# Optimization experiments

Measured on AMD Instinct MI355X. Metric: run time of the kernel, lower is better.

The kernel has to match this reference:

```python
import jax, jax.numpy as jnp
import numpy as np

N = 100000
E = 1600000
H = 128
R = 200
NB = 16  # num_bases (blocks)


def _softplus(x):
    return jax.nn.softplus(x)


def bdd_rel_conv(h, src, dst, etype, norm, W, loop_w, bias, act):
    # W: (R, NB, si, so); block-diagonal decomposition RelGraphConv (DGL semantics)
    nb, si, so = W.shape[1], W.shape[2], W.shape[3]
    h_src = h[src].reshape(-1, nb, si)          # gather per-edge src feats
    W_e = W[etype]                               # (E, nb, si, so) per-edge blocks
    msg = jnp.einsum('ebi,ebio->ebo', h_src, W_e).reshape(-1, nb * so)
    msg = msg * norm                             # edge norm, (E,1)
    agg = jax.ops.segment_sum(msg, dst, num_segments=h.shape[0])
    out = agg + bias + h @ loop_w                # bias + self-loop
    return act(out)


def setup_inputs() -> dict:
    key = jax.random.key(0)
    ks = jax.random.split(key, 12)
    node_ids = jnp.arange(N, dtype=jnp.int32)
    src = jax.random.randint(ks[0], (E,), 0, N)
    dst = jax.random.randint(ks[1], (E,), 0, N)
    etype = jax.random.randint(ks[2], (E,), 0, R)
    norm = jax.random.uniform(ks[3], (E, 1), dtype=jnp.float32)
    emb = jax.random.normal(ks[4], (N, H), dtype=jnp.float32)
    si = H // NB
    W1 = jax.random.normal(ks[5], (R, NB, si, si), dtype=jnp.float32) * 0.05
    loop1 = jax.random.normal(ks[6], (H, H), dtype=jnp.float32) * 0.05
    b1 = jnp.zeros((H,), dtype=jnp.float32)
    W2 = jax.random.normal(ks[7], (R, NB, si, 2 * si), dtype=jnp.float32) * 0.05
    loop2 = jax.random.normal(ks[8], (H, 2 * H), dtype=jnp.float32) * 0.05
    b2 = jnp.zeros((2 * H,), dtype=jnp.float32)
    eps = jax.random.normal(ks[9], (N, H), dtype=jnp.float32)
    return {"node_ids": node_ids, "src": src, "dst": dst, "etype": etype,
            "norm": norm, "emb": emb, "W1": W1, "loop1": loop1, "b1": b1,
            "W2": W2, "loop2": loop2, "b2": b2, "eps": eps}


def reference(node_ids, src, dst, etype, norm, emb, W1, loop1, b1, W2, loop2, b2, eps):
    h = emb[node_ids]                                  # EmbeddingLayer
    h = bdd_rel_conv(h, src, dst, etype, norm, W1, loop1, b1, jax.nn.relu)
    h = bdd_rel_conv(h, src, dst, etype, norm, W2, loop2, b2, lambda x: x)
    m, hv = jnp.split(h, 2, axis=-1)                   # gaussian_parameters
    v = _softplus(hv) + 1e-8
    z = m + jnp.sqrt(v) * eps                          # sample_gaussian
    return z
```

## Files before the change

### kernel.cpp

```cpp
#include <hip/hip_runtime.h>
#include <math.h>

#define N_NODES 100000
#define N_EDGES 1600000
#define HDIM 128
#define NBLK 16
#define NREL 200
#define NW_AGG 8192
#define NT 8

typedef unsigned short ushort_t;
typedef unsigned int uint_t;
typedef _Float16 h2 __attribute__((ext_vector_type(2)));

__device__ __forceinline__ ushort_t f2h(float f) {
  _Float16 h = (_Float16)f;
  return __builtin_bit_cast(unsigned short, h);
}
__device__ __forceinline__ float h2f(ushort_t b) {
  return (float)__builtin_bit_cast(_Float16, b);
}

#if defined(__has_builtin) && __has_builtin(__builtin_amdgcn_fdot2)
#define FDOT2(accv, au, bu)                                                    \
  accv = __builtin_amdgcn_fdot2(__builtin_bit_cast(h2, au),                    \
                                __builtin_bit_cast(h2, bu), accv, false);
#else
#define FDOT2(accv, au, bu)                                                    \
  {                                                                            \
    h2 av_ = __builtin_bit_cast(h2, au);                                       \
    h2 bv_ = __builtin_bit_cast(h2, bu);                                       \
    accv = fmaf((float)av_[0], (float)bv_[0], accv);                           \
    accv = fmaf((float)av_[1], (float)bv_[1], accv);                           \
  }
#endif

#if defined(__has_builtin) && __has_builtin(__builtin_amdgcn_global_load_lds)
#define HAVE_GLL 1
#else
#define HAVE_GLL 0
#endif

#if HAVE_GLL
#define STAGE_H(HSRC, SMEMW)                                                   \
  {                                                                            \
    _Pragma("unroll") for (int i_ = 0; i_ < 8; ++i_) {                         \
      int ei_ = (i_ << 2) + (l >> 4);                                          \
      if (ei_ >= m) ei_ = m - 1;                                               \
      int ss_ = __shfl(r.x, ei_);                                              \
      const ushort_t* gsrc_ = HSRC + ((long)ss_ << 7) + ((l & 15) << 3);       \
      __builtin_amdgcn_global_load_lds(                                        \
          (const __attribute__((address_space(1))) unsigned int*)gsrc_,        \
          (__attribute__((address_space(3))) unsigned int*)&SMEMW[i_ << 9],    \
          16, 0, 0);                                                           \
    }                                                                          \
    asm volatile("s_waitcnt vmcnt(0)" ::: "memory");                           \
  }
#else
#define STAGE_H(HSRC, SMEMW)                                                   \
  {                                                                            \
    _Pragma("unroll") for (int i_ = 0; i_ < 8; ++i_) {                         \
      int ei_ = (i_ << 2) + (l >> 4);                                          \
      if (ei_ >= m) ei_ = m - 1;                                               \
      int ss_ = __shfl(r.x, ei_);                                              \
      const ushort_t* gsrc_ = HSRC + ((long)ss_ << 7) + ((l & 15) << 3);       \
      uint4 t_ = *(const uint4*)gsrc_;                                         \
      *(uint4*)&SMEMW[(i_ << 9) + (l << 3)] = t_;                              \
    }                                                                          \
  }
#endif

__global__ __launch_bounds__(256) void hist_deg(const int* __restrict__ dst,
                                                int* __restrict__ deg) {
  int e = blockIdx.x * 256 + threadIdx.x;
  if (e < N_EDGES) atomicAdd(&deg[dst[e]], 1);
}

__global__ __launch_bounds__(1024) void scan_offsets(const int* __restrict__ deg,
                                                     int* __restrict__ offsets) {
  __shared__ int wsum[16];
  __shared__ int carry_s;
  int tid = threadIdx.x, lane = tid & 63, wid = tid >> 6;
  if (tid == 0) carry_s = 0;
  __syncthreads();
  for (int base = 0; base < N_NODES; base += 1024) {
    int i = base + tid;
    int v = (i < N_NODES) ? deg[i] : 0;
    int x = v;
#pragma unroll
    for (int s = 1; s < 64; s <<= 1) {
      int t = __shfl_up(x, s);
      if (lane >= s) x += t;
    }
    if (lane == 63) wsum[wid] = x;
    __syncthreads();
    if (wid == 0) {
      int y = (lane < 16) ? wsum[lane] : 0;
#pragma unroll
      for (int s = 1; s < 16; s <<= 1) {
        int t = __shfl_up(y, s);
        if (lane >= s) y += t;
      }
      if (lane < 16) wsum[lane] = y;
    }
    __syncthreads();
    int carry = carry_s;
    int wbase = (wid > 0) ? wsum[wid - 1] : 0;
    if (i < N_NODES) offsets[i] = carry + wbase + (x - v);
    __syncthreads();
    if (tid == 0) carry_s = carry + wsum[15];
    __syncthreads();
  }
  if (tid == 0) offsets[N_NODES] = carry_s;
}

__global__ __launch_bounds__(256) void scatter_rec(
    const int* __restrict__ src, const int* __restrict__ dst,
    const int* __restrict__ etype, const float* __restrict__ norm,
    const int* __restrict__ offsets, int* __restrict__ cursor,
    int4* __restrict__ rec) {
  int e = blockIdx.x * 256 + threadIdx.x;
  if (e >= N_EDGES) return;
  int d = dst[e];
  int pos = offsets[d] + atomicAdd(&cursor[d], 1);
  rec[pos] = make_int4(src[e], etype[e], __float_as_int(norm[e]), 0);
}

__global__ __launch_bounds__(256) void calc_ranges(const int* __restrict__ offsets,
                                                   int* __restrict__ ranges) {
  int w = blockIdx.x * 256 + threadIdx.x;
  if (w > NW_AGG) return;
  if (w == NW_AGG) {
    ranges[w] = N_NODES;
    return;
  }
  long t = ((long)w * N_EDGES + NW_AGG - 1) / NW_AGG;
  int lo = 0, hi = N_NODES;
  while (lo < hi) {
    int mid = (lo + hi) >> 1;
    if ((long)offsets[mid] >= t) hi = mid;
    else lo = mid + 1;
  }
  ranges[w] = lo;
}

__global__ __launch_bounds__(256) void conv_h0(const int* __restrict__ node_ids,
                                               const float* __restrict__ emb,
                                               ushort_t* __restrict__ h0h) {
  long gid = (long)blockIdx.x * 256 + threadIdx.x;
  if (gid >= (long)N_NODES * HDIM) return;
  int n = (int)(gid >> 7);
  int o = (int)(gid & 127);
  h0h[gid] = f2h(emb[(long)node_ids[n] * HDIM + o]);
}

__global__ __launch_bounds__(256) void conv_w1(const float* __restrict__ W,
                                               ushort_t* __restrict__ Wh) {
  int idx = blockIdx.x * 256 + threadIdx.x;
  if (idx >= NREL * NBLK * 64) return;
  int rb = idx >> 6, i = (idx >> 3) & 7, o = idx & 7;
  int g = o >> 1, c = o & 1, ip = i >> 1, hi = i & 1;
  Wh[(((rb * 4 + g) * 2 + c) * 4 + ip) * 2 + hi] = f2h(W[idx]);
}

__global__ __launch_bounds__(256) void conv_w2(const float* __restrict__ W,
                                               ushort_t* __restrict__ Wh) {
  int idx = blockIdx.x * 256 + threadIdx.x;
  if (idx >= NREL * NBLK * 128) return;
  int rb = idx >> 7, i = (idx >> 4) & 7, o = idx & 15;
  int g = o >> 2, c = o & 3, ip = i >> 1, hi = i & 1;
  Wh[(((rb * 4 + g) * 4 + c) * 4 + ip) * 2 + hi] = f2h(W[idx]);
}

__global__ __launch_bounds__(256, 4) void agg_layer1(
    const int4* __restrict__ rec, const int* __restrict__ offsets,
    const int* __restrict__ ranges, const ushort_t* __restrict__ h0h,
    const ushort_t* __restrict__ Wh, float* __restrict__ agg) {
  __shared__ __align__(16) ushort_t smem[4][4096];
  int w = blockIdx.x * 4 + (threadIdx.x >> 6);
  int l = threadIdx.x & 63;
  int wid = threadIdx.x >> 6;
  int lo = ranges[w], hi = ranges[w + 1];
  if (lo >= hi) return;
  const ushort_t* Wl = Wh + (size_t)l * 16;
  int hoff = (l >> 2) << 3;
  int estart = offsets[lo];
  int ecnt = offsets[hi] - estart;
  int cur = lo;
  int next_b = offsets[lo + 1];
  int e = estart;
  float ac0 = 0.f, ac1 = 0.f;

#define L1_FLUSH                                                               \
  {                                                                            \
    float2 res = {ac0, ac1};                                                   \
    *(float2*)(agg + (long)cur * HDIM + (l << 1)) = res;                       \
    ac0 = ac1 = 0.f;                                                           \
    ++cur;                                                                     \
    next_b = offsets[cur + 1];                                                 \
  }

  for (int c0 = 0; c0 < ecnt; c0 += 32) {
    int m = min(32, ecnt - c0);
    int4 r = make_int4(0, 0, 0, 0);
    if (l < m) r = rec[estart + c0 + l];
    STAGE_H(h0h, smem[wid])
    for (int k = 0; k < m; ++k) {
      while (e == next_b) L1_FLUSH
      int wy_ = __shfl(r.y, k);
      float nn_ = __uint_as_float((uint_t)__shfl(r.z, k));
      const uint4* Wp_ = (const uint4*)(Wl + (size_t)wy_ * 1024);
      uint4 q0_ = Wp_[0], q1_ = Wp_[1];
      uint4 u = *(const uint4*)&smem[wid][(k << 7) + hoff];
      float p0 = 0.f, p1 = 0.f;
      FDOT2(p0, u.x, q0_.x) FDOT2(p0, u.y, q0_.y)
      FDOT2(p0, u.z, q0_.z) FDOT2(p0, u.w, q0_.w)
      FDOT2(p1, u.x, q1_.x) FDOT2(p1, u.y, q1_.y)
      FDOT2(p1, u.z, q1_.z) FDOT2(p1, u.w, q1_.w)
      ac0 = fmaf(p0, nn_, ac0);
      ac1 = fmaf(p1, nn_, ac1);
      ++e;
    }
  }
  while (cur < hi) {
    float2 res = {ac0, ac1};
    *(float2*)(agg + (long)cur * HDIM + (l << 1)) = res;
    ac0 = ac1 = 0.f;
    ++cur;
  }
#undef L1_FLUSH
}

__global__ __launch_bounds__(256, 4) void agg_layer2(
    const int4* __restrict__ rec, const int* __restrict__ offsets,
    const int* __restrict__ ranges, const ushort_t* __restrict__ h1h,
    const ushort_t* __restrict__ Wh, float* __restrict__ agg) {
  __shared__ __align__(16) ushort_t smem[4][4096];
  int w = blockIdx.x * 4 + (threadIdx.x >> 6);
  int l = threadIdx.x & 63;
  int wid = threadIdx.x >> 6;
  int lo = ranges[w], hi = ranges[w + 1];
  if (lo >= hi) return;
  const ushort_t* Wl = Wh + (size_t)l * 32;
  int hoff = (l >> 2) << 3;
  int estart = offsets[lo];
  int ecnt = offsets[hi] - estart;
  int cur = lo;
  int next_b = offsets[lo + 1];
  int e = estart;
  float ax = 0.f, ay = 0.f, az = 0.f, aw = 0.f;

#define L2_FLUSH                                                               \
  {                                                                            \
    float4 res = {ax, ay, az, aw};                                             \
    *(float4*)(agg + (long)cur * 256 + (l << 2)) = res;                        \
    ax = ay = az = aw = 0.f;                                                   \
    ++cur;                                                                     \
    next_b = offsets[cur + 1];                                                 \
  }

  for (int c0 = 0; c0 < ecnt; c0 += 32) {
    int m = min(32, ecnt - c0);
    int4 r = make_int4(0, 0, 0, 0);
    if (l < m) r = rec[estart + c0 + l];
    STAGE_H(h1h, smem[wid])
    for (int k = 0; k < m; ++k) {
      while (e == next_b) L2_FLUSH
      int wy_ = __shfl(r.y, k);
      float nn_ = __uint_as_float((uint_t)__shfl(r.z, k));
      const uint4* Wp_ = (const uint4*)(Wl + (size_t)wy_ * 2048);
      uint4 q0_ = Wp_[0], q1_ = Wp_[1], q2_ = Wp_[2], q3_ = Wp_[3];
      uint4 u = *(const uint4*)&smem[wid][(k << 7) + hoff];
      float px = 0.f, py = 0.f, pz = 0.f, pw = 0.f;
      FDOT2(px, u.x, q0_.x) FDOT2(px, u.y, q0_.y)
      FDOT2(px, u.z, q0_.z) FDOT2(px, u.w, q0_.w)
      FDOT2(py, u.x, q1_.x) FDOT2(py, u.y, q1_.y)
      FDOT2(py, u.z, q1_.z) FDOT2(py, u.w, q1_.w)
      FDOT2(pz, u.x, q2_.x) FDOT2(pz, u.y, q2_.y)
      FDOT2(pz, u.z, q2_.z) FDOT2(pz, u.w, q2_.w)
      FDOT2(pw, u.x, q3_.x) FDOT2(pw, u.y, q3_.y)
      FDOT2(pw, u.z, q3_.z) FDOT2(pw, u.w, q3_.w)
      ax = fmaf(px, nn_, ax);
      ay = fmaf(py, nn_, ay);
      az = fmaf(pz, nn_, az);
      aw = fmaf(pw, nn_, aw);
      ++e;
    }
  }
  while (cur < hi) {
    float4 res = {ax, ay, az, aw};
    *(float4*)(agg + (long)cur * 256 + (l << 2)) = res;
    ax = ay = az = aw = 0.f;
    ++cur;
  }
#undef L2_FLUSH
}

__global__ __launch_bounds__(256) void node_layer1(
    const ushort_t* __restrict__ h0h, const float* __restrict__ loop1,
    const float* __restrict__ agg1, const float* __restrict__ bias,
    ushort_t* __restrict__ h1h) {
  __shared__ __align__(8) ushort_t Lh[128 * 130];
  __shared__ __align__(8) ushort_t hs[NT * 128];
  int tid = threadIdx.x;
  for (int t = 0; t < 64; ++t) {
    int flat = t * 256 + tid;
    int i = flat >> 7, o = flat & 127;
    Lh[o * 130 + i] = f2h(loop1[i * 128 + o]);
  }
  __syncthreads();
  int o = tid & 127;
  int g = tid >> 7;
  for (int grp = blockIdx.x; grp < N_NODES / NT; grp += gridDim.x) {
    int n0 = grp * NT;
    __syncthreads();
    for (int t = 0; t < 4; ++t) {
      int flat = t * 256 + tid;
      int j = flat >> 7, i = flat & 127;
      hs[j * 128 + i] = h0h[(long)(n0 + j) * 128 + i];
    }
    __syncthreads();
    float acc[4] = {0.f, 0.f, 0.f, 0.f};
    const ushort_t* Lo = &Lh[o * 130];
    const ushort_t* hb = &hs[(g * 4) * 128];
    for (int i = 0; i < 128; i += 4) {
      uint_t lv01 = *(const uint_t*)&Lo[i];
      uint_t lv23 = *(const uint_t*)&Lo[i + 2];
#pragma unroll
      for (int j = 0; j < 4; ++j) {
        uint2 hj = *(const uint2*)&hb[j * 128 + i];
        FDOT2(acc[j], hj.x, lv01)
        FDOT2(acc[j], hj.y, lv23)
      }
    }
    float bo = bias[o];
#pragma unroll
    for (int j = 0; j < 4; ++j) {
      int n = n0 + g * 4 + j;
      float v = acc[j] + bo + agg1[(long)n * 128 + o];
      h1h[(long)n * 128 + o] = f2h(fmaxf(v, 0.f));
    }
  }
}

__global__ __launch_bounds__(256) void node_layer2f(
    const ushort_t* __restrict__ h1h, const float* __restrict__ loop2,
    const float* __restrict__ agg2, const float* __restrict__ bias2,
    const float* __restrict__ eps, float* __restrict__ out) {
  __shared__ __align__(8) ushort_t Lh[256 * 130];
  __shared__ __align__(8) ushort_t hs[NT * 128];
  __shared__ float spbuf[NT * 128];
  int o = threadIdx.x;
  for (int t = 0; t < 128; ++t) {
    int flat = t * 256 + o;
    int i = flat >> 8, c = flat & 255;
    Lh[c * 130 + i] = f2h(loop2[i * 256 + c]);
  }
  __syncthreads();
  for (int grp = blockIdx.x; grp < N_NODES / NT; grp += gridDim.x) {
    int n0 = grp * NT;
    __syncthreads();
    for (int t = 0; t < 4; ++t) {
      int flat = t * 256 + o;
      int j = flat >> 7, i = flat & 127;
      hs[j * 128 + i] = h1h[(long)(n0 + j) * 128 + i];
    }
    __syncthreads();
    float acc[NT] = {0.f, 0.f, 0.f, 0.f, 0.f, 0.f, 0.f, 0.f};
    const ushort_t* Lo = &Lh[o * 130];
    for (int i = 0; i < 128; i += 4) {
      uint_t lv01 = *(const uint_t*)&Lo[i];
      uint_t lv23 = *(const uint_t*)&Lo[i + 2];
#pragma unroll
      for (int j = 0; j < NT; ++j) {
        uint2 hj = *(const uint2*)&hs[j * 128 + i];
        FDOT2(acc[j], hj.x, lv01)
        FDOT2(acc[j], hj.y, lv23)
      }
    }
    float bo = bias2[o];
    if (o >= 128) {
      int oc = o - 128;
#pragma unroll
      for (int j = 0; j < NT; ++j) {
        float hv = acc[j] + bo + agg2[(long)(n0 + j) * 256 + o];
        float sp = fmaxf(hv, 0.f) + log1pf(expf(-fabsf(hv)));
        spbuf[j * 128 + oc] = sqrtf(sp + 1e-8f);
      }
    }
    __syncthreads();
    if (o < 128) {
#pragma unroll
      for (int j = 0; j < NT; ++j) {
        float mval = acc[j] + bo + agg2[(long)(n0 + j) * 256 + o];
        long off2 = (long)(n0 + j) * 128 + o;
        out[off2] = mval + spbuf[j * 128 + o] * eps[off2];
      }
    }
  }
}

extern "C" void kernel_launch(void* const* d_in, const int* in_sizes, int n_in,
                              void* d_out, int out_size, void* d_ws, size_t ws_size,
                              hipStream_t stream) {
  const int* node_ids = (const int*)d_in[0];
  const int* src      = (const int*)d_in[1];
  const int* dst      = (const int*)d_in[2];
  const int* etype    = (const int*)d_in[3];
  const float* norm   = (const float*)d_in[4];
  const float* emb    = (const float*)d_in[5];
  const float* W1     = (const float*)d_in[6];
  const float* loop1  = (const float*)d_in[7];
  const float* b1     = (const float*)d_in[8];
  const float* W2     = (const float*)d_in[9];
  const float* loop2  = (const float*)d_in[10];
  const float* b2     = (const float*)d_in[11];
  const float* eps    = (const float*)d_in[12];
  float* out = (float*)d_out;

  char* ws = (char*)d_ws;
  size_t off = 0;
  int* deg       = (int*)(ws + off); off += (size_t)N_NODES * 4;
  int* offsets   = (int*)(ws + off); off += (size_t)(N_NODES + 1) * 4;
  int* cursor    = (int*)(ws + off); off += (size_t)N_NODES * 4;
  int* ranges    = (int*)(ws + off); off += (size_t)(NW_AGG + 1) * 4;
  int4* rec      = (int4*)(ws + off); off += (size_t)N_EDGES * 16;
  float* agg2    = (float*)(ws + off); off += (size_t)N_NODES * 256 * 4;
  ushort_t* h0h  = (ushort_t*)(ws + off); off += (size_t)N_NODES * HDIM * 2;
  ushort_t* h1h  = (ushort_t*)(ws + off); off += (size_t)N_NODES * HDIM * 2;
  ushort_t* Wh1  = (ushort_t*)(ws + off); off += (size_t)NREL * NBLK * 64 * 2;
  ushort_t* Wh2  = (ushort_t*)(ws + off); off += (size_t)NREL * NBLK * 128 * 2;
  float* agg1 = out;

  hipMemsetAsync(deg, 0, (size_t)N_NODES * 4, stream);
  hipMemsetAsync(cursor, 0, (size_t)N_NODES * 4, stream);
  hist_deg<<<(N_EDGES + 255) / 256, 256, 0, stream>>>(dst, deg);
  conv_w1<<<(NREL * NBLK * 64 + 255) / 256, 256, 0, stream>>>(W1, Wh1);
  conv_w2<<<(NREL * NBLK * 128 + 255) / 256, 256, 0, stream>>>(W2, Wh2);
  scan_offsets<<<1, 1024, 0, stream>>>(deg, offsets);
  calc_ranges<<<(NW_AGG + 256) / 256, 256, 0, stream>>>(offsets, ranges);
  scatter_rec<<<(N_EDGES + 255) / 256, 256, 0, stream>>>(src, dst, etype, norm,
                                                         offsets, cursor, rec);
  conv_h0<<<(N_NODES * HDIM + 255) / 256, 256, 0, stream>>>(node_ids, emb, h0h);

  agg_layer1<<<NW_AGG / 4, 256, 0, stream>>>(rec, offsets, ranges, h0h, Wh1, agg1);
  node_layer1<<<1024, 256, 0, stream>>>(h0h, loop1, agg1, b1, h1h);

  agg_layer2<<<NW_AGG / 4, 256, 0, stream>>>(rec, offsets, ranges, h1h, Wh2, agg2);
  node_layer2f<<<512, 256, 0, stream>>>(h1h, loop2, agg2, b2, eps, out);
}
```

Measured before the change: 1.151 ms.

## Sort edges by relation, materialize per-edge messages, then reduce per destination node

Adds a second edge ordering grouped by relation type, so the message kernels load each relation's weight block once into registers and process 64-edge tiles. Each kernel writes fp16 messages into a per-edge buffer indexed by the edge's CSR position. The node kernels then sum those messages per destination while applying the self-loop and activation. This removes the per-edge weight gather from the old destination-ordered aggregation, at the cost of writing and re-reading a large message buffer (up to 800 MB) and adding extra histogram, scan and scatter passes. The new path runs only if the workspace is large enough; otherwise the old path is kept.

```diff
diff --git a/kernel.cpp b/kernel.cpp
--- a/kernel.cpp
+++ b/kernel.cpp
@@ -7,6 +7,7 @@
 #define NBLK 16
 #define NREL 200
 #define NW_AGG 8192
+#define TILE_E 64
 #define NT 8
 
 typedef unsigned short ushort_t;
@@ -42,7 +43,7 @@
 #endif
 
 #if HAVE_GLL
-#define STAGE_H(HSRC, SMEMW)                                                   \
+#define STAGE_H32(HSRC, SMEMW)                                                 \
   {                                                                            \
     _Pragma("unroll") for (int i_ = 0; i_ < 8; ++i_) {                         \
       int ei_ = (i_ << 2) + (l >> 4);                                          \
@@ -57,7 +58,7 @@
     asm volatile("s_waitcnt vmcnt(0)" ::: "memory");                           \
   }
 #else
-#define STAGE_H(HSRC, SMEMW)                                                   \
+#define STAGE_H32(HSRC, SMEMW)                                                 \
   {                                                                            \
     _Pragma("unroll") for (int i_ = 0; i_ < 8; ++i_) {                         \
       int ei_ = (i_ << 2) + (l >> 4);                                          \
@@ -70,10 +71,45 @@
   }
 #endif
 
+#if HAVE_GLL
+#define STAGE16R(HSRC, SLABP, RR, MM, LL)                                      \
+  {                                                                            \
+    _Pragma("unroll") for (int i_ = 0; i_ < 4; ++i_) {                         \
+      int ei_ = (i_ << 2) + (LL >> 4);                                         \
+      if (ei_ >= MM) ei_ = MM - 1;                                             \
+      int ss_ = __shfl(RR.x, ei_);                                             \
+      const ushort_t* gsrc_ = HSRC + ((long)ss_ << 7) + ((LL & 15) << 3);      \
+      __builtin_amdgcn_global_load_lds(                                        \
+          (const __attribute__((address_space(1))) unsigned int*)gsrc_,        \
+          (__attribute__((address_space(3))) unsigned int*)&SLABP[i_ << 9],    \
+          16, 0, 0);                                                           \
+    }                                                                          \
+    asm volatile("s_waitcnt vmcnt(0)" ::: "memory");                           \
+  }
+#else
+#define STAGE16R(HSRC, SLABP, RR, MM, LL)                                      \
+  {                                                                            \
+    _Pragma("unroll") for (int i_ = 0; i_ < 4; ++i_) {                         \
+      int ei_ = (i_ << 2) + (LL >> 4);                                         \
+      if (ei_ >= MM) ei_ = MM - 1;                                             \
+      int ss_ = __shfl(RR.x, ei_);                                             \
+      const ushort_t* gsrc_ = HSRC + ((long)ss_ << 7) + ((LL & 15) << 3);      \
+      uint4 t_ = *(const uint4*)gsrc_;                                         \
+      *(uint4*)&SLABP[(i_ << 9) + (LL << 3)] = t_;                             \
+    }                                                                          \
+  }
+#endif
+
 __global__ __launch_bounds__(256) void hist_deg(const int* __restrict__ dst,
                                                 int* __restrict__ deg) {
   int e = blockIdx.x * 256 + threadIdx.x;
   if (e < N_EDGES) atomicAdd(&deg[dst[e]], 1);
+}
+
+__global__ __launch_bounds__(256) void hist_rel(const int* __restrict__ etype,
+                                                int* __restrict__ cnt2) {
+  int e = blockIdx.x * 256 + threadIdx.x;
+  if (e < N_EDGES) atomicAdd(&cnt2[etype[e]], 1);
 }
 
 __global__ __launch_bounds__(1024) void scan_offsets(const int* __restrict__ deg,
@@ -114,6 +150,37 @@
   if (tid == 0) offsets[N_NODES] = carry_s;
 }
 
+__global__ __launch_bounds__(256) void scan_rel(const int* __restrict__ cnt2,
+                                                int* __restrict__ off2,
+                                                int* __restrict__ tileOff) {
+  __shared__ int b1[256], b2[256];
+  int t = threadIdx.x;
+  int c = (t < NREL) ? cnt2[t] : 0;
+  int tc = (c + TILE_E - 1) / TILE_E;
+  int x1 = c, x2 = tc;
+  b1[t] = x1;
+  b2[t] = x2;
+  __syncthreads();
+  for (int s = 1; s < 256; s <<= 1) {
+    int a1 = (t >= s) ? b1[t - s] : 0;
+    int a2 = (t >= s) ? b2[t - s] : 0;
+    __syncthreads();
+    x1 += a1;
+    x2 += a2;
+    b1[t] = x1;
+    b2[t] = x2;
+    __syncthreads();
+  }
+  if (t < NREL) {
+    off2[t] = x1 - c;
+    tileOff[t] = x2 - tc;
+  }
+  if (t == NREL - 1) {
+    off2[NREL] = x1;
+    tileOff[NREL] = x2;
+  }
+}
+
 __global__ __launch_bounds__(256) void scatter_rec(
     const int* __restrict__ src, const int* __restrict__ dst,
     const int* __restrict__ etype, const float* __restrict__ norm,
@@ -124,6 +191,21 @@
   int d = dst[e];
   int pos = offsets[d] + atomicAdd(&cursor[d], 1);
   rec[pos] = make_int4(src[e], etype[e], __float_as_int(norm[e]), 0);
+}
+
+__global__ __launch_bounds__(256) void scatter2(
+    const int* __restrict__ src, const int* __restrict__ dst,
+    const int* __restrict__ etype, const float* __restrict__ norm,
+    const int* __restrict__ offsets, int* __restrict__ cursor,
+    const int* __restrict__ off2, int* __restrict__ cur2,
+    int4* __restrict__ rec2) {
+  int e = blockIdx.x * 256 + threadIdx.x;
+  if (e >= N_EDGES) return;
+  int d = dst[e];
+  int pc = offsets[d] + atomicAdd(&cursor[d], 1);
+  int rr = etype[e];
+  int pr = off2[rr] + atomicAdd(&cur2[rr], 1);
+  rec2[pr] = make_int4(src[e], pc, __float_as_int(norm[e]), 0);
 }
 
 __global__ __launch_bounds__(256) void calc_ranges(const int* __restrict__ offsets,
@@ -190,7 +272,6 @@
   int next_b = offsets[lo + 1];
   int e = estart;
   float ac0 = 0.f, ac1 = 0.f;
-
 #define L1_FLUSH                                                               \
   {                                                                            \
     float2 res = {ac0, ac1};                                                   \
@@ -199,12 +280,11 @@
     ++cur;                                                                     \
     next_b = offsets[cur + 1];                                                 \
   }
-
   for (int c0 = 0; c0 < ecnt; c0 += 32) {
     int m = min(32, ecnt - c0);
     int4 r = make_int4(0, 0, 0, 0);
     if (l < m) r = rec[estart + c0 + l];
-    STAGE_H(h0h, smem[wid])
+    STAGE_H32(h0h, smem[wid])
     for (int k = 0; k < m; ++k) {
       while (e == next_b) L1_FLUSH
       int wy_ = __shfl(r.y, k);
@@ -249,7 +329,6 @@
   int next_b = offsets[lo + 1];
   int e = estart;
   float ax = 0.f, ay = 0.f, az = 0.f, aw = 0.f;
-
 #define L2_FLUSH                                                               \
   {                                                                            \
     float4 res = {ax, ay, az, aw};                                             \
@@ -258,12 +337,11 @@
     ++cur;                                                                     \
     next_b = offsets[cur + 1];                                                 \
   }
-
   for (int c0 = 0; c0 < ecnt; c0 += 32) {
     int m = min(32, ecnt - c0);
     int4 r = make_int4(0, 0, 0, 0);
     if (l < m) r = rec[estart + c0 + l];
-    STAGE_H(h1h, smem[wid])
+    STAGE_H32(h1h, smem[wid])
     for (int k = 0; k < m; ++k) {
       while (e == next_b) L2_FLUSH
       int wy_ = __shfl(r.y, k);
@@ -296,6 +374,102 @@
 #undef L2_FLUSH
 }
 
+__global__ __launch_bounds__(256, 4) void msg_gemm1(
+    const int4* __restrict__ rec2, const int* __restrict__ off2,
+    const int* __restrict__ tileOff, const ushort_t* __restrict__ h0h,
+    const ushort_t* __restrict__ Wh, ushort_t* __restrict__ msg) {
+  __shared__ __align__(16) ushort_t smem[4][2048];
+  int b = blockIdx.x;
+  if (b >= tileOff[NREL]) return;
+  int lo = 0, hi = NREL;
+  while (lo + 1 < hi) {
+    int mid = (lo + hi) >> 1;
+    if (tileOff[mid] <= b) lo = mid;
+    else hi = mid;
+  }
+  int rrel = lo;
+  int t = b - tileOff[rrel];
+  int ebase = off2[rrel] + t * TILE_E;
+  int m64 = off2[rrel + 1] - off2[rrel] - t * TILE_E;
+  if (m64 > TILE_E) m64 = TILE_E;
+  int wid = threadIdx.x >> 6, l = threadIdx.x & 63;
+  int mw = m64 - wid * 16;
+  mw = mw < 0 ? 0 : (mw > 16 ? 16 : mw);
+  if (mw <= 0) return;
+  const uint4* Wp = (const uint4*)(Wh + (size_t)rrel * 1024 + (size_t)l * 16);
+  uint4 q0 = Wp[0], q1 = Wp[1];
+  int4 r2 = make_int4(0, 0, 0, 0);
+  if (l < mw) r2 = rec2[ebase + wid * 16 + l];
+  STAGE16R(h0h, smem[wid], r2, mw, l)
+  int hoff = (l >> 2) << 3;
+  for (int k = 0; k < mw; ++k) {
+    int p = __shfl(r2.y, k);
+    float nn = __uint_as_float((uint_t)__shfl(r2.z, k));
+    uint4 u = *(const uint4*)&smem[wid][(k << 7) + hoff];
+    float p0 = 0.f, p1 = 0.f;
+    FDOT2(p0, u.x, q0.x) FDOT2(p0, u.y, q0.y)
+    FDOT2(p0, u.z, q0.z) FDOT2(p0, u.w, q0.w)
+    FDOT2(p1, u.x, q1.x) FDOT2(p1, u.y, q1.y)
+    FDOT2(p1, u.z, q1.z) FDOT2(p1, u.w, q1.w)
+    p0 *= nn;
+    p1 *= nn;
+    uint_t ov = (uint_t)f2h(p0) | ((uint_t)f2h(p1) << 16);
+    *(uint_t*)&msg[(long)p * 128 + (l << 1)] = ov;
+  }
+}
+
+__global__ __launch_bounds__(256, 4) void msg_gemm2(
+    const int4* __restrict__ rec2, const int* __restrict__ off2,
+    const int* __restrict__ tileOff, const ushort_t* __restrict__ h1h,
+    const ushort_t* __restrict__ Wh, ushort_t* __restrict__ msg) {
+  __shared__ __align__(16) ushort_t smem[4][2048];
+  int b = blockIdx.x;
+  if (b >= tileOff[NREL]) return;
+  int lo = 0, hi = NREL;
+  while (lo + 1 < hi) {
+    int mid = (lo + hi) >> 1;
+    if (tileOff[mid] <= b) lo = mid;
+    else hi = mid;
+  }
+  int rrel = lo;
+  int t = b - tileOff[rrel];
+  int ebase = off2[rrel] + t * TILE_E;
+  int m64 = off2[rrel + 1] - off2[rrel] - t * TILE_E;
+  if (m64 > TILE_E) m64 = TILE_E;
+  int wid = threadIdx.x >> 6, l = threadIdx.x & 63;
+  int mw = m64 - wid * 16;
+  mw = mw < 0 ? 0 : (mw > 16 ? 16 : mw);
+  if (mw <= 0) return;
+  const uint4* Wp = (const uint4*)(Wh + (size_t)rrel * 2048 + (size_t)l * 32);
+  uint4 q0 = Wp[0], q1 = Wp[1], q2 = Wp[2], q3 = Wp[3];
+  int4 r2 = make_int4(0, 0, 0, 0);
+  if (l < mw) r2 = rec2[ebase + wid * 16 + l];
+  STAGE16R(h1h, smem[wid], r2, mw, l)
+  int hoff = (l >> 2) << 3;
+  for (int k = 0; k < mw; ++k) {
+    int p = __shfl(r2.y, k);
+    float nn = __uint_as_float((uint_t)__shfl(r2.z, k));
+    uint4 u = *(const uint4*)&smem[wid][(k << 7) + hoff];
+    float px = 0.f, py = 0.f, pz = 0.f, pw = 0.f;
+    FDOT2(px, u.x, q0.x) FDOT2(px, u.y, q0.y)
+    FDOT2(px, u.z, q0.z) FDOT2(px, u.w, q0.w)
+    FDOT2(py, u.x, q1.x) FDOT2(py, u.y, q1.y)
+    FDOT2(py, u.z, q1.z) FDOT2(py, u.w, q1.w)
+    FDOT2(pz, u.x, q2.x) FDOT2(pz, u.y, q2.y)
+    FDOT2(pz, u.z, q2.z) FDOT2(pz, u.w, q2.w)
+    FDOT2(pw, u.x, q3.x) FDOT2(pw, u.y, q3.y)
+    FDOT2(pw, u.z, q3.z) FDOT2(pw, u.w, q3.w)
+    px *= nn;
+    py *= nn;
+    pz *= nn;
+    pw *= nn;
+    uint2 ov;
+    ov.x = (uint_t)f2h(px) | ((uint_t)f2h(py) << 16);
+    ov.y = (uint_t)f2h(pz) | ((uint_t)f2h(pw) << 16);
+    *(uint2*)&msg[(long)p * 256 + (l << 2)] = ov;
+  }
+}
+
 __global__ __launch_bounds__(256) void node_layer1(
     const ushort_t* __restrict__ h0h, const float* __restrict__ loop1,
     const float* __restrict__ agg1, const float* __restrict__ bias,
@@ -393,8 +567,123 @@
 #pragma unroll
       for (int j = 0; j < NT; ++j) {
         float mval = acc[j] + bo + agg2[(long)(n0 + j) * 256 + o];
-        long off2 = (long)(n0 + j) * 128 + o;
-        out[off2] = mval + spbuf[j * 128 + o] * eps[off2];
+        long off2_ = (long)(n0 + j) * 128 + o;
+        out[off2_] = mval + spbuf[j * 128 + o] * eps[off2_];
+      }
+    }
+  }
+}
+
+__global__ __launch_bounds__(256) void node_layer1m(
+    const ushort_t* __restrict__ h0h, const float* __restrict__ loop1,
+    const ushort_t* __restrict__ msg1, const int* __restrict__ offsets,
+    const float* __restrict__ bias, ushort_t* __restrict__ h1h) {
+  __shared__ __align__(8) ushort_t Lh[128 * 130];
+  __shared__ __align__(8) ushort_t hs[NT * 128];
+  int tid = threadIdx.x;
+  for (int t = 0; t < 64; ++t) {
+    int flat = t * 256 + tid;
+    int i = flat >> 7, o = flat & 127;
+    Lh[o * 130 + i] = f2h(loop1[i * 128 + o]);
+  }
+  __syncthreads();
+  int o = tid & 127;
+  int g = tid >> 7;
+  for (int grp = blockIdx.x; grp < N_NODES / NT; grp += gridDim.x) {
+    int n0 = grp * NT;
+    __syncthreads();
+    for (int t = 0; t < 4; ++t) {
+      int flat = t * 256 + tid;
+      int j = flat >> 7, i = flat & 127;
+      hs[j * 128 + i] = h0h[(long)(n0 + j) * 128 + i];
+    }
+    __syncthreads();
+    float acc[4] = {0.f, 0.f, 0.f, 0.f};
+    const ushort_t* Lo = &Lh[o * 130];
+    const ushort_t* hb = &hs[(g * 4) * 128];
+    for (int i = 0; i < 128; i += 4) {
+      uint_t lv01 = *(const uint_t*)&Lo[i];
+      uint_t lv23 = *(const uint_t*)&Lo[i + 2];
+#pragma unroll
+      for (int j = 0; j < 4; ++j) {
+        uint2 hj = *(const uint2*)&hb[j * 128 + i];
+        FDOT2(acc[j], hj.x, lv01)
+        FDOT2(acc[j], hj.y, lv23)
+      }
+    }
+    float bo = bias[o];
+#pragma unroll
+    for (int j = 0; j < 4; ++j) {
+      int n = n0 + g * 4 + j;
+      int s = offsets[n], eN = offsets[n + 1];
+      float ag = 0.f;
+      for (int k = s; k < eN; ++k) ag += h2f(msg1[(long)k * 128 + o]);
+      float v = acc[j] + bo + ag;
+      h1h[(long)n * 128 + o] = f2h(fmaxf(v, 0.f));
+    }
+  }
+}
+
+__global__ __launch_bounds__(256) void node_layer2fm(
+    const ushort_t* __restrict__ h1h, const float* __restrict__ loop2,
+    const ushort_t* __restrict__ msg2, const int* __restrict__ offsets,
+    const float* __restrict__ bias2, const float* __restrict__ eps,
+    float* __restrict__ out) {
+  __shared__ __align__(8) ushort_t Lh[256 * 130];
+  __shared__ __align__(8) ushort_t hs[NT * 128];
+  __shared__ float spbuf[NT * 128];
+  int o = threadIdx.x;
+  for (int t = 0; t < 128; ++t) {
+    int flat = t * 256 + o;
+    int i = flat >> 8, c = flat & 255;
+    Lh[c * 130 + i] = f2h(loop2[i * 256 + c]);
+  }
+  __syncthreads();
+  for (int grp = blockIdx.x; grp < N_NODES / NT; grp += gridDim.x) {
+    int n0 = grp * NT;
+    __syncthreads();
+    for (int t = 0; t < 4; ++t) {
+      int flat = t * 256 + o;
+      int j = flat >> 7, i = flat & 127;
+      hs[j * 128 + i] = h1h[(long)(n0 + j) * 128 + i];
+    }
+    __syncthreads();
+    float acc[NT] = {0.f, 0.f, 0.f, 0.f, 0.f, 0.f, 0.f, 0.f};
+    const ushort_t* Lo = &Lh[o * 130];
+    for (int i = 0; i < 128; i += 4) {
+      uint_t lv01 = *(const uint_t*)&Lo[i];
+      uint_t lv23 = *(const uint_t*)&Lo[i + 2];
+#pragma unroll
+      for (int j = 0; j < NT; ++j) {
+        uint2 hj = *(const uint2*)&hs[j * 128 + i];
+        FDOT2(acc[j], hj.x, lv01)
+        FDOT2(acc[j], hj.y, lv23)
+      }
+    }
+    float bo = bias2[o];
+#pragma unroll
+    for (int j = 0; j < NT; ++j) {
+      int n = n0 + j;
+      int s = offsets[n], eN = offsets[n + 1];
+      float ag = 0.f;
+      for (int k = s; k < eN; ++k) ag += h2f(msg2[(long)k * 256 + o]);
+      acc[j] += bo + ag;
+    }
+    if (o >= 128) {
+      int oc = o - 128;
+#pragma unroll
+      for (int j = 0; j < NT; ++j) {
+        float hv = acc[j];
+        float sp = fmaxf(hv, 0.f) + log1pf(expf(-fabsf(hv)));
+        spbuf[j * 128 + oc] = sqrtf(sp + 1e-8f);
+      }
+    }
+    __syncthreads();
+    if (o < 128) {
+#pragma unroll
+      for (int j = 0; j < NT; ++j) {
+        long off2_ = (long)(n0 + j) * 128 + o;
+        out[off2_] = acc[j] + spbuf[j * 128 + o] * eps[off2_];
       }
     }
   }
@@ -420,32 +709,55 @@
 
   char* ws = (char*)d_ws;
   size_t off = 0;
-  int* deg       = (int*)(ws + off); off += (size_t)N_NODES * 4;
-  int* offsets   = (int*)(ws + off); off += (size_t)(N_NODES + 1) * 4;
-  int* cursor    = (int*)(ws + off); off += (size_t)N_NODES * 4;
-  int* ranges    = (int*)(ws + off); off += (size_t)(NW_AGG + 1) * 4;
-  int4* rec      = (int4*)(ws + off); off += (size_t)N_EDGES * 16;
-  float* agg2    = (float*)(ws + off); off += (size_t)N_NODES * 256 * 4;
-  ushort_t* h0h  = (ushort_t*)(ws + off); off += (size_t)N_NODES * HDIM * 2;
-  ushort_t* h1h  = (ushort_t*)(ws + off); off += (size_t)N_NODES * HDIM * 2;
-  ushort_t* Wh1  = (ushort_t*)(ws + off); off += (size_t)NREL * NBLK * 64 * 2;
-  ushort_t* Wh2  = (ushort_t*)(ws + off); off += (size_t)NREL * NBLK * 128 * 2;
-  float* agg1 = out;
-
-  hipMemsetAsync(deg, 0, (size_t)N_NODES * 4, stream);
-  hipMemsetAsync(cursor, 0, (size_t)N_NODES * 4, stream);
+  int* deg     = (int*)(ws + off); off += (size_t)N_NODES * 4;
+  int* cursor  = (int*)(ws + off); off += (size_t)N_NODES * 4;
+  int* cnt2    = (int*)(ws + off); off += 256 * 4;
+  int* cur2    = (int*)(ws + off); off += 256 * 4;
+  int* offsets = (int*)(ws + off); off += (size_t)(N_NODES + 1) * 4;
+  int* off2    = (int*)(ws + off); off += 256 * 4;
+  int* tileOff = (int*)(ws + off); off += 256 * 4;
+  int* ranges  = (int*)(ws + off); off += (size_t)(NW_AGG + 1) * 4;
+  off = (off + 15) & ~(size_t)15;
+  int4* rec     = (int4*)(ws + off); off += (size_t)N_EDGES * 16;
+  ushort_t* h0h = (ushort_t*)(ws + off); off += (size_t)N_NODES * HDIM * 2;
+  ushort_t* h1h = (ushort_t*)(ws + off); off += (size_t)N_NODES * HDIM * 2;
+  ushort_t* Wh1 = (ushort_t*)(ws + off); off += (size_t)NREL * NBLK * 64 * 2;
+  ushort_t* Wh2 = (ushort_t*)(ws + off); off += (size_t)NREL * NBLK * 128 * 2;
+  off = (off + 15) & ~(size_t)15;
+  size_t tail = off;
+  size_t need_msg = tail + (size_t)N_EDGES * 256 * 2;
+  size_t need_fb  = tail + (size_t)N_NODES * 256 * 4;
+  bool use_msg = (ws_size >= need_msg);
+
+  hipMemsetAsync(deg, 0, ((size_t)2 * N_NODES + 512) * 4, stream);
   hist_deg<<<(N_EDGES + 255) / 256, 256, 0, stream>>>(dst, deg);
   conv_w1<<<(NREL * NBLK * 64 + 255) / 256, 256, 0, stream>>>(W1, Wh1);
   conv_w2<<<(NREL * NBLK * 128 + 255) / 256, 256, 0, stream>>>(W2, Wh2);
   scan_offsets<<<1, 1024, 0, stream>>>(deg, offsets);
-  calc_ranges<<<(NW_AGG + 256) / 256, 256, 0, stream>>>(offsets, ranges);
-  scatter_rec<<<(N_EDGES + 255) / 256, 256, 0, stream>>>(src, dst, etype, norm,
-                                                         offsets, cursor, rec);
   conv_h0<<<(N_NODES * HDIM + 255) / 256, 256, 0, stream>>>(node_ids, emb, h0h);
 
-  agg_layer1<<<NW_AGG / 4, 256, 0, stream>>>(rec, offsets, ranges, h0h, Wh1, agg1);
-  node_layer1<<<1024, 256, 0, stream>>>(h0h, loop1, agg1, b1, h1h);
-
-  agg_layer2<<<NW_AGG / 4, 256, 0, stream>>>(rec, offsets, ranges, h1h, Wh2, agg2);
-  node_layer2f<<<512, 256, 0, stream>>>(h1h, loop2, agg2, b2, eps, out);
-}
+  if (use_msg) {
+    ushort_t* msg = (ushort_t*)(ws + tail);
+    const int T_MAX = N_EDGES / TILE_E + NREL;
+    hist_rel<<<(N_EDGES + 255) / 256, 256, 0, stream>>>(etype, cnt2);
+    scan_rel<<<1, 256, 0, stream>>>(cnt2, off2, tileOff);
+    scatter2<<<(N_EDGES + 255) / 256, 256, 0, stream>>>(src, dst, etype, norm,
+                                                        offsets, cursor, off2,
+                                                        cur2, rec);
+    msg_gemm1<<<T_MAX, 256, 0, stream>>>(rec, off2, tileOff, h0h, Wh1, msg);
+    node_layer1m<<<1024, 256, 0, stream>>>(h0h, loop1, msg, offsets, b1, h1h);
+    msg_gemm2<<<T_MAX, 256, 0, stream>>>(rec, off2, tileOff, h1h, Wh2, msg);
+    node_layer2fm<<<512, 256, 0, stream>>>(h1h, loop2, msg, offsets, b2, eps, out);
+  } else {
+    float* agg2 = (float*)(ws + tail);
+    float* agg1 = out;
+    (void)need_fb;
+    calc_ranges<<<(NW_AGG + 256) / 256, 256, 0, stream>>>(offsets, ranges);
+    scatter_rec<<<(N_EDGES + 255) / 256, 256, 0, stream>>>(src, dst, etype, norm,
+                                                           offsets, cursor, rec);
+    agg_layer1<<<NW_AGG / 4, 256, 0, stream>>>(rec, offsets, ranges, h0h, Wh1, agg1);
+    node_layer1<<<1024, 256, 0, stream>>>(h0h, loop1, agg1, b1, h1h);
+    agg_layer2<<<NW_AGG / 4, 256, 0, stream>>>(rec, offsets, ranges, h1h, Wh2, agg2);
+    node_layer2f<<<512, 256, 0, stream>>>(h1h, loop2, agg2, b2, eps, out);
+  }
+}
```

Result: no change. 1.132 ms (-1.6%).
